# Performance work log

Measured on AMD Instinct MI355X. Metric: run time of the kernel, lower is better.

The kernel has to match this reference:

```python
import jax, jax.numpy as jnp
import numpy as np

GAMMA = 0.99   # discount_factor
LAM = 0.95     # smoothing_factor

def setup_inputs() -> dict:
    key = jax.random.key(0)
    k1, k2, k3, k4 = jax.random.split(key, 4)
    B, T = 4096, 2048
    return {
        "rewards": jax.random.normal(k1, (B, T), dtype=jnp.float32),
        "values": jax.random.normal(k2, (B, T), dtype=jnp.float32),
        "next_value": jax.random.normal(k3, (B,), dtype=jnp.float32),
        "done_flags": jax.random.randint(k4, (B, T), 0, 2, dtype=jnp.int32),
    }

def reference(rewards, values, next_value, done_flags):
    d = done_flags.astype(rewards.dtype)
    # next_non_terminal[t] = 1 - done[t+1] for t < T-1, and 1 - done[T-1] at t = T-1
    nnt = 1.0 - jnp.concatenate([d[..., 1:], d[..., -1:]], axis=-1)
    # next value at step t: values[t+1] for t < T-1, bootstrap next_value at t = T-1
    nv = jnp.concatenate([values[..., 1:], next_value[..., None]], axis=-1)
    delta = rewards + GAMMA * nv * nnt - values  # [B, T]

    def step(gae, x):
        dl, nn = x
        gae = dl + GAMMA * LAM * nn * gae
        return gae, gae

    # scan backward over time (leading axis for lax.scan)
    deltaT = jnp.moveaxis(delta, -1, 0)  # [T, B]
    nntT = jnp.moveaxis(nnt, -1, 0)      # [T, B]
    init = jnp.zeros(rewards.shape[:-1], rewards.dtype)
    _, advT = jax.lax.scan(step, init, (deltaT, nntT), reverse=True)
    advantages = jnp.moveaxis(advT, 0, -1)  # [B, T]
    returns = advantages + values
    return advantages, returns
```

## Files before the change

### kernel.cpp

```cpp
#include <hip/hip_runtime.h>

#define GAMMA 0.99f
#define LAM   0.95f

typedef float v4f __attribute__((ext_vector_type(4)));
typedef int   v4i __attribute__((ext_vector_type(4)));

constexpr int LCHUNK = 32;
constexpr int WPB    = 4;

__global__ __launch_bounds__(256, 4) void gae_wave_kernel(
    const float* __restrict__ rewards,
    const float* __restrict__ values,
    const float* __restrict__ next_value,
    const int*   __restrict__ done,
    float* __restrict__ adv_out,
    float* __restrict__ ret_out,
    int B, int T)
{
    const int tid  = threadIdx.x;
    const int lane = tid & 63;
    const int wave = tid >> 6;
    const int row  = blockIdx.x * WPB + wave;
    if (row >= B) return;

    const long rowbase = (long)row * T;
    const int  col0    = lane * LCHUNK;

    float rr[LCHUNK], vv[LCHUNK];
    int   dd[LCHUNK];
    {
        const v4f* gr = reinterpret_cast<const v4f*>(rewards + rowbase + col0);
        const v4f* gv = reinterpret_cast<const v4f*>(values  + rowbase + col0);
        const v4i* gd = reinterpret_cast<const v4i*>(done    + rowbase + col0);
        v4f* R4 = reinterpret_cast<v4f*>(rr);
        v4f* V4 = reinterpret_cast<v4f*>(vv);
        v4i* D4 = reinterpret_cast<v4i*>(dd);
#pragma unroll
        for (int k = 0; k < LCHUNK / 4; ++k) R4[k] = gr[k];
#pragma unroll
        for (int k = 0; k < LCHUNK / 4; ++k) V4[k] = gv[k];
#pragma unroll
        for (int k = 0; k < LCHUNK / 4; ++k) D4[k] = gd[k];
    }
    const float nvrow = next_value[row];

    int   dnext = __shfl_down(dd[0], 1);
    float vnext = __shfl_down(vv[0], 1);
    if (lane == 63) {
        dnext = dd[LCHUNK - 1];
        vnext = nvrow;
    }

    unsigned mask = 0;
#pragma unroll
    for (int j = 0; j < LCHUNK - 1; ++j)
        mask |= (dd[j + 1] ? 1u : 0u) << j;
    mask |= (dnext ? 1u : 0u) << (LCHUNK - 1);

    float delta[LCHUNK];
#pragma unroll
    for (int j = 0; j < LCHUNK; ++j) {
        const float nnt = ((mask >> j) & 1u) ? 0.0f : 1.0f;
        const float nv  = (j < LCHUNK - 1) ? vv[j + 1] : vnext;
        delta[j] = rr[j] + GAMMA * nv * nnt - vv[j];
    }

    float a = 0.0f, m = 1.0f;
#pragma unroll
    for (int j = LCHUNK - 1; j >= 0; --j) {
        const float c = ((mask >> j) & 1u) ? 0.0f : (GAMMA * LAM);
        a = delta[j] + c * a;
        m = c * m;
    }

    float sa = a, sm = m;
#pragma unroll
    for (int d = 1; d < 64; d <<= 1) {
        float oa = __shfl_down(sa, d);
        float om = __shfl_down(sm, d);
        if (lane + d < 64) { sa = sa + sm * oa; sm = sm * om; }
    }
    float gin = __shfl_down(sa, 1);
    if (lane == 63) gin = 0.0f;

#pragma unroll
    for (int j = LCHUNK - 1; j >= 0; --j) {
        const float c = ((mask >> j) & 1u) ? 0.0f : (GAMMA * LAM);
        gin = delta[j] + c * gin;
        delta[j] = gin;
    }

    v4f* a4 = reinterpret_cast<v4f*>(adv_out + rowbase + col0);
    v4f* t4 = reinterpret_cast<v4f*>(ret_out + rowbase + col0);
    const v4f* A4 = reinterpret_cast<const v4f*>(delta);
#pragma unroll
    for (int k = 0; k < LCHUNK / 4; ++k) a4[k] = A4[k];
#pragma unroll
    for (int k = 0; k < LCHUNK / 4; ++k) {
        v4f s;
        s.x = delta[4 * k + 0] + vv[4 * k + 0];
        s.y = delta[4 * k + 1] + vv[4 * k + 1];
        s.z = delta[4 * k + 2] + vv[4 * k + 2];
        s.w = delta[4 * k + 3] + vv[4 * k + 3];
        t4[k] = s;
    }
}

__global__ void gae_naive_kernel(
    const float* __restrict__ rewards,
    const float* __restrict__ values,
    const float* __restrict__ next_value,
    const int*   __restrict__ done,
    float* __restrict__ adv_out,
    float* __restrict__ ret_out,
    int B, int T)
{
    int row = blockIdx.x * blockDim.x + threadIdx.x;
    if (row >= B) return;
    long base = (long)row * T;
    float g = 0.0f;
    for (int t = T - 1; t >= 0; --t) {
        int dcol = (t + 1 < T) ? (t + 1) : (T - 1);
        float nnt = 1.0f - (float)done[base + dcol];
        float nv  = (t + 1 < T) ? values[base + t + 1] : next_value[row];
        float dl  = rewards[base + t] + GAMMA * nv * nnt - values[base + t];
        g = dl + (GAMMA * LAM) * nnt * g;
        adv_out[base + t] = g;
        ret_out[base + t] = g + values[base + t];
    }
}

extern "C" void kernel_launch(void* const* d_in, const int* in_sizes, int n_in,
                              void* d_out, int out_size, void* d_ws, size_t ws_size,
                              hipStream_t stream) {
    const float* rewards    = (const float*)d_in[0];
    const float* values     = (const float*)d_in[1];
    const float* next_value = (const float*)d_in[2];
    const int*   done       = (const int*)d_in[3];

    const int B = in_sizes[2];
    const int T = in_sizes[0] / B;

    float* adv = (float*)d_out;
    float* ret = adv + (long)B * T;

    if (T == 64 * LCHUNK) {
        const int grid = (B + WPB - 1) / WPB;
        gae_wave_kernel<<<grid, 256, 0, stream>>>(
            rewards, values, next_value, done, adv, ret, B, T);
    } else {
        gae_naive_kernel<<<(B + 255) / 256, 256, 0, stream>>>(
            rewards, values, next_value, done, adv, ret, B, T);
    }
}
```

Baseline: 164.5 us.

## Split each row into four wave segments with coalesced loads and carried scan state

```diff
diff --git a/kernel.cpp b/kernel.cpp
--- a/kernel.cpp
+++ b/kernel.cpp
@@ -6,10 +6,93 @@
 typedef float v4f __attribute__((ext_vector_type(4)));
 typedef int   v4i __attribute__((ext_vector_type(4)));
 
-constexpr int LCHUNK = 32;
-constexpr int WPB    = 4;
+constexpr int CH   = 8;
+constexpr int SEG  = 64 * CH;
+constexpr int NSEG = 4;
+constexpr int WPB  = 4;
 
-__global__ __launch_bounds__(256, 4) void gae_wave_kernel(
+struct Raw {
+    v4f ra, rb, va, vb;
+    v4i da, db;
+};
+
+__device__ __forceinline__ Raw load_seg(const float* __restrict__ r,
+                                        const float* __restrict__ v,
+                                        const int*   __restrict__ d,
+                                        long base) {
+    Raw x;
+    x.ra = reinterpret_cast<const v4f*>(r + base)[0];
+    x.rb = reinterpret_cast<const v4f*>(r + base)[1];
+    x.va = reinterpret_cast<const v4f*>(v + base)[0];
+    x.vb = reinterpret_cast<const v4f*>(v + base)[1];
+    x.da = reinterpret_cast<const v4i*>(d + base)[0];
+    x.db = reinterpret_cast<const v4i*>(d + base)[1];
+    return x;
+}
+
+__device__ __forceinline__ void compute_seg(
+    const Raw x, const int lane, const bool last_seg, const float nvrow,
+    float& g, float& bv, int& bd,
+    float* __restrict__ adv_out, float* __restrict__ ret_out, const long base)
+{
+    float r[CH] = {x.ra.x, x.ra.y, x.ra.z, x.ra.w, x.rb.x, x.rb.y, x.rb.z, x.rb.w};
+    float v[CH] = {x.va.x, x.va.y, x.va.z, x.va.w, x.vb.x, x.vb.y, x.vb.z, x.vb.w};
+    int   d[CH] = {x.da.x, x.da.y, x.da.z, x.da.w, x.db.x, x.db.y, x.db.z, x.db.w};
+
+    int   dnext = __shfl_down(d[0], 1);
+    float vnext = __shfl_down(v[0], 1);
+    if (lane == 63) {
+        dnext = last_seg ? d[CH - 1] : bd;
+        vnext = last_seg ? nvrow     : bv;
+    }
+    const float bv_new = __shfl(v[0], 0);
+    const int   bd_new = __shfl(d[0], 0);
+
+    float delta[CH], c[CH];
+#pragma unroll
+    for (int j = 0; j < CH; ++j) {
+        const int   dn  = (j < CH - 1) ? d[j + 1] : dnext;
+        const float nv  = (j < CH - 1) ? v[j + 1] : vnext;
+        const float nnt = dn ? 0.0f : 1.0f;
+        delta[j] = r[j] + GAMMA * nv * nnt - v[j];
+        c[j]     = dn ? 0.0f : (GAMMA * LAM);
+    }
+
+    float a = 0.0f, m = 1.0f;
+#pragma unroll
+    for (int j = CH - 1; j >= 0; --j) { a = delta[j] + c[j] * a; m = c[j] * m; }
+
+    float sa = a, sm = m;
+#pragma unroll
+    for (int s = 1; s < 64; s <<= 1) {
+        const float oa = __shfl_down(sa, s);
+        const float om = __shfl_down(sm, s);
+        if (lane + s < 64) { sa += sm * oa; sm *= om; }
+    }
+    float gin = __shfl_down(sa, 1);
+    float em  = __shfl_down(sm, 1);
+    if (lane == 63) { gin = 0.0f; em = 1.0f; }
+    gin = gin + em * g;
+
+    float adv[CH];
+#pragma unroll
+    for (int j = CH - 1; j >= 0; --j) { gin = delta[j] + c[j] * gin; adv[j] = gin; }
+
+    v4f* a4 = reinterpret_cast<v4f*>(adv_out + base);
+    v4f* t4 = reinterpret_cast<v4f*>(ret_out + base);
+    v4f o0; o0.x = adv[0]; o0.y = adv[1]; o0.z = adv[2]; o0.w = adv[3];
+    v4f o1; o1.x = adv[4]; o1.y = adv[5]; o1.z = adv[6]; o1.w = adv[7];
+    v4f s0; s0.x = adv[0]+v[0]; s0.y = adv[1]+v[1]; s0.z = adv[2]+v[2]; s0.w = adv[3]+v[3];
+    v4f s1; s1.x = adv[4]+v[4]; s1.y = adv[5]+v[5]; s1.z = adv[6]+v[6]; s1.w = adv[7]+v[7];
+    a4[0] = o0; a4[1] = o1;
+    t4[0] = s0; t4[1] = s1;
+
+    g  = __shfl(gin, 0);
+    bv = bv_new;
+    bd = bd_new;
+}
+
+__global__ __launch_bounds__(256, 4) void gae_wave_seg_kernel(
     const float* __restrict__ rewards,
     const float* __restrict__ values,
     const float* __restrict__ next_value,
@@ -25,86 +108,21 @@
     if (row >= B) return;
 
     const long rowbase = (long)row * T;
-    const int  col0    = lane * LCHUNK;
+    const long laneoff = rowbase + lane * CH;
 
-    float rr[LCHUNK], vv[LCHUNK];
-    int   dd[LCHUNK];
-    {
-        const v4f* gr = reinterpret_cast<const v4f*>(rewards + rowbase + col0);
-        const v4f* gv = reinterpret_cast<const v4f*>(values  + rowbase + col0);
-        const v4i* gd = reinterpret_cast<const v4i*>(done    + rowbase + col0);
-        v4f* R4 = reinterpret_cast<v4f*>(rr);
-        v4f* V4 = reinterpret_cast<v4f*>(vv);
-        v4i* D4 = reinterpret_cast<v4i*>(dd);
-#pragma unroll
-        for (int k = 0; k < LCHUNK / 4; ++k) R4[k] = gr[k];
-#pragma unroll
-        for (int k = 0; k < LCHUNK / 4; ++k) V4[k] = gv[k];
-#pragma unroll
-        for (int k = 0; k < LCHUNK / 4; ++k) D4[k] = gd[k];
-    }
+    Raw b3 = load_seg(rewards, values, done, laneoff + 3 * SEG);
+    Raw b2 = load_seg(rewards, values, done, laneoff + 2 * SEG);
     const float nvrow = next_value[row];
 
-    int   dnext = __shfl_down(dd[0], 1);
-    float vnext = __shfl_down(vv[0], 1);
-    if (lane == 63) {
-        dnext = dd[LCHUNK - 1];
-        vnext = nvrow;
-    }
+    float g = 0.0f, bv = 0.0f;
+    int   bd = 0;
 
-    unsigned mask = 0;
-#pragma unroll
-    for (int j = 0; j < LCHUNK - 1; ++j)
-        mask |= (dd[j + 1] ? 1u : 0u) << j;
-    mask |= (dnext ? 1u : 0u) << (LCHUNK - 1);
-
-    float delta[LCHUNK];
-#pragma unroll
-    for (int j = 0; j < LCHUNK; ++j) {
-        const float nnt = ((mask >> j) & 1u) ? 0.0f : 1.0f;
-        const float nv  = (j < LCHUNK - 1) ? vv[j + 1] : vnext;
-        delta[j] = rr[j] + GAMMA * nv * nnt - vv[j];
-    }
-
-    float a = 0.0f, m = 1.0f;
-#pragma unroll
-    for (int j = LCHUNK - 1; j >= 0; --j) {
-        const float c = ((mask >> j) & 1u) ? 0.0f : (GAMMA * LAM);
-        a = delta[j] + c * a;
-        m = c * m;
-    }
-
-    float sa = a, sm = m;
-#pragma unroll
-    for (int d = 1; d < 64; d <<= 1) {
-        float oa = __shfl_down(sa, d);
-        float om = __shfl_down(sm, d);
-        if (lane + d < 64) { sa = sa + sm * oa; sm = sm * om; }
-    }
-    float gin = __shfl_down(sa, 1);
-    if (lane == 63) gin = 0.0f;
-
-#pragma unroll
-    for (int j = LCHUNK - 1; j >= 0; --j) {
-        const float c = ((mask >> j) & 1u) ? 0.0f : (GAMMA * LAM);
-        gin = delta[j] + c * gin;
-        delta[j] = gin;
-    }
-
-    v4f* a4 = reinterpret_cast<v4f*>(adv_out + rowbase + col0);
-    v4f* t4 = reinterpret_cast<v4f*>(ret_out + rowbase + col0);
-    const v4f* A4 = reinterpret_cast<const v4f*>(delta);
-#pragma unroll
-    for (int k = 0; k < LCHUNK / 4; ++k) a4[k] = A4[k];
-#pragma unroll
-    for (int k = 0; k < LCHUNK / 4; ++k) {
-        v4f s;
-        s.x = delta[4 * k + 0] + vv[4 * k + 0];
-        s.y = delta[4 * k + 1] + vv[4 * k + 1];
-        s.z = delta[4 * k + 2] + vv[4 * k + 2];
-        s.w = delta[4 * k + 3] + vv[4 * k + 3];
-        t4[k] = s;
-    }
+    Raw b1 = load_seg(rewards, values, done, laneoff + 1 * SEG);
+    compute_seg(b3, lane, true,  nvrow, g, bv, bd, adv_out, ret_out, laneoff + 3 * SEG);
+    Raw b0 = load_seg(rewards, values, done, laneoff + 0 * SEG);
+    compute_seg(b2, lane, false, nvrow, g, bv, bd, adv_out, ret_out, laneoff + 2 * SEG);
+    compute_seg(b1, lane, false, nvrow, g, bv, bd, adv_out, ret_out, laneoff + 1 * SEG);
+    compute_seg(b0, lane, false, nvrow, g, bv, bd, adv_out, ret_out, laneoff + 0 * SEG);
 }
 
 __global__ void gae_naive_kernel(
@@ -145,9 +163,9 @@
     float* adv = (float*)d_out;
     float* ret = adv + (long)B * T;
 
-    if (T == 64 * LCHUNK) {
+    if (T == NSEG * SEG) {
         const int grid = (B + WPB - 1) / WPB;
-        gae_wave_kernel<<<grid, 256, 0, stream>>>(
+        gae_wave_seg_kernel<<<grid, 256, 0, stream>>>(
             rewards, values, next_value, done, adv, ret, B, T);
     } else {
         gae_naive_kernel<<<(B + 255) / 256, 256, 0, stream>>>(
```

Result: faster. 153.2 us (-6.9%).
